# Kernel optimization log

Measured on AMD Instinct MI355X. Metric: run time of the kernel, lower is better.

The kernel has to match this reference:

```python
import jax, jax.numpy as jnp
import numpy as np

D_MODEL = 512
NUM_HEADS = 8
DEPTH = D_MODEL // NUM_HEADS
BATCH = 16
SEQ = 1024


def setup_inputs() -> dict:
    key = jax.random.key(0)
    kq, kk, kv, k1, k2, k3, k4 = jax.random.split(key, 7)
    scale = 1.0 / np.sqrt(D_MODEL)
    return {
        "v": jax.random.normal(kv, (BATCH, SEQ, D_MODEL), jnp.float32),
        "k": jax.random.normal(kk, (BATCH, SEQ, D_MODEL), jnp.float32),
        "q": jax.random.normal(kq, (BATCH, SEQ, D_MODEL), jnp.float32),
        "mask": jnp.ones((BATCH, SEQ), jnp.float32),
        # Conv1D(kernel_size=1, use_bias=False) == per-token Linear: x @ W, W [d_in, d_out]
        "Wq": jax.random.normal(k1, (D_MODEL, D_MODEL), jnp.float32) * scale,
        "Wk": jax.random.normal(k2, (D_MODEL, D_MODEL), jnp.float32) * scale,
        "Wv": jax.random.normal(k3, (D_MODEL, D_MODEL), jnp.float32) * scale,
        "Wo": jax.random.normal(k4, (D_MODEL, D_MODEL), jnp.float32) * scale,
    }


def _split_heads(x, batch):
    # [b, s, d_model] -> [b, h, s, depth]
    return x.reshape(batch, -1, NUM_HEADS, DEPTH).transpose(0, 2, 1, 3)


def reference(v, k, q, mask, Wq, Wk, Wv, Wo):
    batch = q.shape[0]
    qh = _split_heads(q @ Wq, batch)  # [b,h,sq,dh]
    kh = _split_heads(k @ Wk, batch)  # [b,h,sk,dh]
    vh = _split_heads(v @ Wv, batch)  # [b,h,sk,dh]

    dk = jnp.asarray(DEPTH, qh.dtype)
    logits = jnp.einsum("bhqd,bhkd->bhqk", qh, kh) / jnp.sqrt(dk)
    # additive padding mask, broadcast [b,1,1,sk]
    logits = logits + (1.0 - mask[:, None, None, :]) * (-1e9)
    attention_weights = jax.nn.softmax(logits, axis=-1)  # [b,h,sq,sk]

    ctx = jnp.einsum("bhqk,bhkd->bhqd", attention_weights, vh)
    ctx = ctx.transpose(0, 2, 1, 3).reshape(batch, -1, D_MODEL)
    output = ctx @ Wo
    return output, attention_weights
```

## Files before the change

### kernel.cpp

```cpp
#include <hip/hip_runtime.h>


typedef _Float16 f16;
typedef _Float16 f16x8 __attribute__((ext_vector_type(8)));
typedef float f32x4 __attribute__((ext_vector_type(4)));

#define DEVINL __device__ __forceinline__

static constexpr int BATCH = 16, SEQ = 1024, DM = 512, NH = 8, DH = 64;

DEVINL void async16(void* lds, const void* g) {
  __builtin_amdgcn_global_load_lds(
      (const __attribute__((address_space(1))) unsigned int*)g,
      (__attribute__((address_space(3))) unsigned int*)lds, 16, 0, 0);
}

__global__ __launch_bounds__(256) void prep_wt_k(
    const float* __restrict__ Wq, const float* __restrict__ Wk,
    const float* __restrict__ Wv, const float* __restrict__ Wo,
    f16* __restrict__ WT) {
  __shared__ float t[32][33];
  const int w = blockIdx.z;
  const float* src = (w == 0) ? Wq : (w == 1) ? Wk : (w == 2) ? Wv : Wo;
  const int k0 = blockIdx.y * 32, n0 = blockIdx.x * 32;
  const int r0 = threadIdx.x >> 5, c = threadIdx.x & 31;
#pragma unroll
  for (int i = 0; i < 4; ++i)
    t[i * 8 + r0][c] = src[(size_t)(k0 + i * 8 + r0) * DM + n0 + c];
  __syncthreads();
  f16* dst = WT + (size_t)w * DM * DM;
#pragma unroll
  for (int i = 0; i < 4; ++i)
    dst[(size_t)(n0 + i * 8 + r0) * DM + k0 + c] = (f16)t[c][i * 8 + r0];
}

template <int MODE>
DEVINL void gemm_body(const float* __restrict__ A32, const f16* __restrict__ A16,
                      const f16* __restrict__ WTn, f16* __restrict__ O16,
                      float* __restrict__ O32) {
  __shared__ __align__(16) f16 As[128 * 32];
  __shared__ __align__(16) f16 Bs[128 * 32];
  const int tid = threadIdx.x;
  const int lane = tid & 63, wave = tid >> 6;
  const int wr = wave >> 1, wc = wave & 1;
  const int m0 = blockIdx.x * 128, n0 = blockIdx.y * 128;
  const int lrow = lane & 15, lkg = lane >> 4;
  f32x4 acc[4][4] = {};

  for (int kt = 0; kt < DM / 32; ++kt) {
    const int k0 = kt * 32;
#pragma unroll
    for (int it = 0; it < 2; ++it) {
      const int o = (it * 256 + tid) * 16;
      const int n = o >> 6, kb = o & 63;
      async16((char*)Bs + (it * 256 + wave * 64) * 16,
              (const char*)WTn + ((size_t)(n0 + n) * DM + k0) * 2 + kb);
    }
    if (MODE == 0) {
      const int row = tid >> 1, kh = (tid & 1) * 16;
      const float* s = A32 + (size_t)(m0 + row) * DM + k0 + kh;
#pragma unroll
      for (int half = 0; half < 2; ++half) {
        f32x4 v0 = *(const f32x4*)(s + half * 8);
        f32x4 v1 = *(const f32x4*)(s + half * 8 + 4);
        f16x8 t;
        t[0] = (f16)v0[0]; t[1] = (f16)v0[1]; t[2] = (f16)v0[2]; t[3] = (f16)v0[3];
        t[4] = (f16)v1[0]; t[5] = (f16)v1[1]; t[6] = (f16)v1[2]; t[7] = (f16)v1[3];
        *(f16x8*)&As[row * 32 + kh + half * 8] = t;
      }
    } else {
#pragma unroll
      for (int it = 0; it < 2; ++it) {
        const int o = (it * 256 + tid) * 16;
        const int row = o >> 6, kb = o & 63;
        async16((char*)As + (it * 256 + wave * 64) * 16,
                (const char*)A16 + ((size_t)(m0 + row) * DM + k0) * 2 + kb);
      }
    }
    __syncthreads();
    f16x8 af[4], bf[4];
#pragma unroll
    for (int i = 0; i < 4; ++i)
      af[i] = *(const f16x8*)&As[(wr * 64 + i * 16 + lrow) * 32 + lkg * 8];
#pragma unroll
    for (int j = 0; j < 4; ++j)
      bf[j] = *(const f16x8*)&Bs[(wc * 64 + j * 16 + lrow) * 32 + lkg * 8];
#pragma unroll
    for (int i = 0; i < 4; ++i)
#pragma unroll
      for (int j = 0; j < 4; ++j)
        acc[i][j] = __builtin_amdgcn_mfma_f32_16x16x32_f16(af[i], bf[j], acc[i][j], 0, 0, 0);
    __syncthreads();
  }

#pragma unroll
  for (int i = 0; i < 4; ++i) {
#pragma unroll
    for (int j = 0; j < 4; ++j) {
#pragma unroll
      for (int r = 0; r < 4; ++r) {
        const int m = m0 + wr * 64 + i * 16 + lkg * 4 + r;
        const int g = n0 + wc * 64 + j * 16 + lrow;
        if (MODE == 0) {
          const int b = m >> 10, s = m & 1023, hh = g >> 6, d = g & 63;
          O16[(((size_t)b * NH + hh) * SEQ + s) * DH + d] = (f16)acc[i][j][r];
        } else {
          O32[(size_t)m * DM + g] = acc[i][j][r];
        }
      }
    }
  }
}

__global__ __launch_bounds__(256, 2) void proj_k(
    const float* __restrict__ q, const float* __restrict__ k, const float* __restrict__ v,
    const f16* __restrict__ WT, f16* __restrict__ Qh, f16* __restrict__ Kh,
    f16* __restrict__ Vh) {
  const int z = blockIdx.z;
  const float* A = (z == 0) ? q : (z == 1) ? k : v;
  const f16* W = WT + (size_t)z * DM * DM;
  f16* O = (z == 0) ? Qh : (z == 1) ? Kh : Vh;
  gemm_body<0>(A, nullptr, W, O, nullptr);
}

__global__ __launch_bounds__(256, 2) void outp_k(const f16* __restrict__ ctx,
                                                 const f16* __restrict__ WoT,
                                                 float* __restrict__ out0) {
  gemm_body<1>(nullptr, ctx, WoT, nullptr, out0);
}

__global__ __launch_bounds__(256, 2) void attn_k(
    const f16* __restrict__ Qh, const f16* __restrict__ Kh, const f16* __restrict__ Vh,
    const float* __restrict__ mask, float* __restrict__ attnW, f16* __restrict__ ctx) {
  __shared__ __align__(16) f16 Ks[64 * 64];
  __shared__ __align__(16) f16 Vt[64 * 64];
  __shared__ __align__(16) f16 Ps[4][16 * 64];
  const int tid = threadIdx.x;
  const int lane = tid & 63, wave = tid >> 6;
  const int lrow = lane & 15, lkg = lane >> 4;
  const int qt = blockIdx.x, h = blockIdx.y, b = blockIdx.z;
  const size_t bh = (size_t)b * NH + h;
  const f16* Kbase = Kh + bh * SEQ * DH;
  const f16* Vbase = Vh + bh * SEQ * DH;
  const int q0 = qt * 64 + wave * 16;

  f16x8 aQ0, aQ1;
  {
    const f16* qp = Qh + (bh * SEQ + q0 + lrow) * DH + lkg * 8;
    aQ0 = *(const f16x8*)qp;
    aQ1 = *(const f16x8*)(qp + 32);
  }

  float sums[4] = {0.f, 0.f, 0.f, 0.f};

  for (int kt = 0; kt < 16; ++kt) {
    const char* KtileB = (const char*)(Kbase + (size_t)kt * 64 * DH);
#pragma unroll
    for (int it = 0; it < 2; ++it) {
      const int o = (it * 256 + tid) * 16;
      const int key = o >> 7, slot = (o >> 4) & 7;
      async16((char*)Ks + (it * 256 + wave * 64) * 16,
              KtileB + key * 128 + ((slot ^ (key & 7)) << 4));
    }
    __syncthreads();
    f32x4 lg[4] = {};
#pragma unroll
    for (int j = 0; j < 4; ++j) {
      const int key = j * 16 + lrow;
      f16x8 b0 = *(const f16x8*)((const char*)Ks + key * 128 + ((lkg ^ (key & 7)) << 4));
      f16x8 b1 = *(const f16x8*)((const char*)Ks + key * 128 + (((4 + lkg) ^ (key & 7)) << 4));
      lg[j] = __builtin_amdgcn_mfma_f32_16x16x32_f16(aQ0, b0, lg[j], 0, 0, 0);
      lg[j] = __builtin_amdgcn_mfma_f32_16x16x32_f16(aQ1, b1, lg[j], 0, 0, 0);
    }
#pragma unroll
    for (int j = 0; j < 4; ++j) {
      const int key = kt * 64 + j * 16 + lrow;
      const float bias = (1.0f - mask[b * SEQ + key]) * (-1e9f);
#pragma unroll
      for (int r = 0; r < 4; ++r) sums[r] += __expf(lg[j][r] * 0.125f + bias);
    }
    __syncthreads();
  }

#pragma unroll
  for (int r = 0; r < 4; ++r) {
    float s = sums[r];
    s += __shfl_xor(s, 1);
    s += __shfl_xor(s, 2);
    s += __shfl_xor(s, 4);
    s += __shfl_xor(s, 8);
    sums[r] = 1.0f / s;
  }

  f32x4 ctxacc[4] = {};
  float* awBase = attnW + (bh * SEQ + q0) * SEQ;

  for (int kt = 0; kt < 16; ++kt) {
    const char* KtileB = (const char*)(Kbase + (size_t)kt * 64 * DH);
#pragma unroll
    for (int it = 0; it < 2; ++it) {
      const int o = (it * 256 + tid) * 16;
      const int key = o >> 7, slot = (o >> 4) & 7;
      async16((char*)Ks + (it * 256 + wave * 64) * 16,
              KtileB + key * 128 + ((slot ^ (key & 7)) << 4));
    }
    {
      const int key = tid >> 2, d0 = (tid & 3) * 16;
      const f16* vp = Vbase + ((size_t)kt * 64 + key) * DH + d0;
      f16x8 v0 = *(const f16x8*)vp;
      f16x8 v1 = *(const f16x8*)(vp + 8);
#pragma unroll
      for (int jj = 0; jj < 8; ++jj) {
        const int d = d0 + jj;
        *(f16*)((char*)Vt + d * 128 + (((key >> 3) ^ (d & 7)) << 4) + (key & 7) * 2) = v0[jj];
      }
#pragma unroll
      for (int jj = 0; jj < 8; ++jj) {
        const int d = d0 + 8 + jj;
        *(f16*)((char*)Vt + d * 128 + (((key >> 3) ^ (d & 7)) << 4) + (key & 7) * 2) = v1[jj];
      }
    }
    __syncthreads();
    f32x4 lg[4] = {};
#pragma unroll
    for (int j = 0; j < 4; ++j) {
      const int key = j * 16 + lrow;
      f16x8 b0 = *(const f16x8*)((const char*)Ks + key * 128 + ((lkg ^ (key & 7)) << 4));
      f16x8 b1 = *(const f16x8*)((const char*)Ks + key * 128 + (((4 + lkg) ^ (key & 7)) << 4));
      lg[j] = __builtin_amdgcn_mfma_f32_16x16x32_f16(aQ0, b0, lg[j], 0, 0, 0);
      lg[j] = __builtin_amdgcn_mfma_f32_16x16x32_f16(aQ1, b1, lg[j], 0, 0, 0);
    }
    float* aw = awBase + kt * 64;
#pragma unroll
    for (int j = 0; j < 4; ++j) {
      const int keyc = j * 16 + lrow;
      const float bias = (1.0f - mask[b * SEQ + kt * 64 + keyc]) * (-1e9f);
#pragma unroll
      for (int r = 0; r < 4; ++r) {
        const int row = lkg * 4 + r;
        const float w = __expf(lg[j][r] * 0.125f + bias) * sums[r];
        aw[(size_t)row * SEQ + keyc] = w;
        *(f16*)((char*)&Ps[wave][0] + row * 128 + (((keyc >> 3) ^ (row & 7)) << 4) +
                (keyc & 7) * 2) = (f16)w;
      }
    }
#pragma unroll
    for (int kk = 0; kk < 2; ++kk) {
      const int kidx = kk * 32 + lkg * 8;
      f16x8 aP = *(const f16x8*)((const char*)&Ps[wave][0] + lrow * 128 +
                                 (((kidx >> 3) ^ (lrow & 7)) << 4));
#pragma unroll
      for (int j2 = 0; j2 < 4; ++j2) {
        const int d = j2 * 16 + lrow;
        f16x8 bV = *(const f16x8*)((const char*)Vt + d * 128 + (((kidx >> 3) ^ (d & 7)) << 4));
        ctxacc[j2] = __builtin_amdgcn_mfma_f32_16x16x32_f16(aP, bV, ctxacc[j2], 0, 0, 0);
      }
    }
    __syncthreads();
  }

#pragma unroll
  for (int j2 = 0; j2 < 4; ++j2)
#pragma unroll
    for (int r = 0; r < 4; ++r) {
      const int s = q0 + lkg * 4 + r;
      const int d = j2 * 16 + lrow;
      ctx[(((size_t)b * SEQ + s) * NH + h) * DH + d] = (f16)ctxacc[j2][r];
    }
}

extern "C" void kernel_launch(void* const* d_in, const int* in_sizes, int n_in,
                              void* d_out, int out_size, void* d_ws, size_t ws_size,
                              hipStream_t stream) {
  const float* v = (const float*)d_in[0];
  const float* k = (const float*)d_in[1];
  const float* q = (const float*)d_in[2];
  const float* mask = (const float*)d_in[3];
  const float* Wq = (const float*)d_in[4];
  const float* Wk = (const float*)d_in[5];
  const float* Wv = (const float*)d_in[6];
  const float* Wo = (const float*)d_in[7];

  float* out0 = (float*)d_out;
  float* attnW = out0 + (size_t)BATCH * SEQ * DM;

  char* ws = (char*)d_ws;
  f16* WT = (f16*)ws;
  f16* Qh = (f16*)(ws + (size_t)4 * DM * DM * 2);
  f16* Kh = Qh + (size_t)BATCH * NH * SEQ * DH;
  f16* Vh = Kh + (size_t)BATCH * NH * SEQ * DH;
  f16* ctx = Vh + (size_t)BATCH * NH * SEQ * DH;

  prep_wt_k<<<dim3(16, 16, 4), 256, 0, stream>>>(Wq, Wk, Wv, Wo, WT);
  proj_k<<<dim3(128, 4, 3), 256, 0, stream>>>(q, k, v, WT, Qh, Kh, Vh);
  attn_k<<<dim3(16, NH, BATCH), 256, 0, stream>>>(Qh, Kh, Vh, mask, attnW, ctx);
  outp_k<<<dim3(128, 4), 256, 0, stream>>>(ctx, WT + (size_t)3 * DM * DM, out0);
}
```

Before: 313.2 us.

## Double-buffer LDS tiles in GEMMs and attention, remap blocks for XCD locality

Adds double-buffered LDS staging to the projection GEMMs and to both attention passes. The next K/V or A/B tile is prefetched, asynchronously or into registers, while MFMAs run on the current one, which also drops one barrier per iteration. Launches become 1D grids whose block ids are remapped so consecutive work lands on the same XCD (bid&7 striding), aiming for better L2 reuse of K/V and weights. LDS use doubles, which could reduce occupancy. The attention kernel is likely dominated by the 64MB attention-weight writes, which limits what overlap can gain.

```diff
diff --git a/kernel.cpp b/kernel.cpp
--- a/kernel.cpp
+++ b/kernel.cpp
@@ -37,59 +37,85 @@
 template <int MODE>
 DEVINL void gemm_body(const float* __restrict__ A32, const f16* __restrict__ A16,
                       const f16* __restrict__ WTn, f16* __restrict__ O16,
-                      float* __restrict__ O32) {
-  __shared__ __align__(16) f16 As[128 * 32];
-  __shared__ __align__(16) f16 Bs[128 * 32];
+                      float* __restrict__ O32, int m0, int n0) {
+  __shared__ __align__(16) f16 As[2][128 * 32];
+  __shared__ __align__(16) f16 Bs[2][128 * 32];
   const int tid = threadIdx.x;
   const int lane = tid & 63, wave = tid >> 6;
   const int wr = wave >> 1, wc = wave & 1;
-  const int m0 = blockIdx.x * 128, n0 = blockIdx.y * 128;
   const int lrow = lane & 15, lkg = lane >> 4;
   f32x4 acc[4][4] = {};
 
-  for (int kt = 0; kt < DM / 32; ++kt) {
-    const int k0 = kt * 32;
+  f32x4 ar[4];
+
+  auto stageB = [&](int kt, int buf) {
 #pragma unroll
     for (int it = 0; it < 2; ++it) {
       const int o = (it * 256 + tid) * 16;
       const int n = o >> 6, kb = o & 63;
-      async16((char*)Bs + (it * 256 + wave * 64) * 16,
-              (const char*)WTn + ((size_t)(n0 + n) * DM + k0) * 2 + kb);
-    }
-    if (MODE == 0) {
-      const int row = tid >> 1, kh = (tid & 1) * 16;
-      const float* s = A32 + (size_t)(m0 + row) * DM + k0 + kh;
-#pragma unroll
-      for (int half = 0; half < 2; ++half) {
-        f32x4 v0 = *(const f32x4*)(s + half * 8);
-        f32x4 v1 = *(const f32x4*)(s + half * 8 + 4);
-        f16x8 t;
-        t[0] = (f16)v0[0]; t[1] = (f16)v0[1]; t[2] = (f16)v0[2]; t[3] = (f16)v0[3];
-        t[4] = (f16)v1[0]; t[5] = (f16)v1[1]; t[6] = (f16)v1[2]; t[7] = (f16)v1[3];
-        *(f16x8*)&As[row * 32 + kh + half * 8] = t;
-      }
-    } else {
-#pragma unroll
-      for (int it = 0; it < 2; ++it) {
-        const int o = (it * 256 + tid) * 16;
-        const int row = o >> 6, kb = o & 63;
-        async16((char*)As + (it * 256 + wave * 64) * 16,
-                (const char*)A16 + ((size_t)(m0 + row) * DM + k0) * 2 + kb);
-      }
-    }
-    __syncthreads();
+      async16((char*)&Bs[buf][0] + (it * 256 + wave * 64) * 16,
+              (const char*)WTn + ((size_t)(n0 + n) * DM + kt * 32) * 2 + kb);
+    }
+  };
+  auto stageA_async = [&](int kt, int buf) {
+#pragma unroll
+    for (int it = 0; it < 2; ++it) {
+      const int o = (it * 256 + tid) * 16;
+      const int row = o >> 6, kb = o & 63;
+      async16((char*)&As[buf][0] + (it * 256 + wave * 64) * 16,
+              (const char*)A16 + ((size_t)(m0 + row) * DM + kt * 32) * 2 + kb);
+    }
+  };
+  auto loadA = [&](int kt) {
+    const int row = tid >> 1, kh = (tid & 1) * 16;
+    const float* s = A32 + (size_t)(m0 + row) * DM + kt * 32 + kh;
+    ar[0] = *(const f32x4*)(s);
+    ar[1] = *(const f32x4*)(s + 4);
+    ar[2] = *(const f32x4*)(s + 8);
+    ar[3] = *(const f32x4*)(s + 12);
+  };
+  auto writeA = [&](int buf) {
+    const int row = tid >> 1, kh = (tid & 1) * 16;
+#pragma unroll
+    for (int half = 0; half < 2; ++half) {
+      f16x8 t;
+      t[0] = (f16)ar[half * 2][0]; t[1] = (f16)ar[half * 2][1];
+      t[2] = (f16)ar[half * 2][2]; t[3] = (f16)ar[half * 2][3];
+      t[4] = (f16)ar[half * 2 + 1][0]; t[5] = (f16)ar[half * 2 + 1][1];
+      t[6] = (f16)ar[half * 2 + 1][2]; t[7] = (f16)ar[half * 2 + 1][3];
+      *(f16x8*)&As[buf][row * 32 + kh + half * 8] = t;
+    }
+  };
+
+  stageB(0, 0);
+  if (MODE == 0) {
+    loadA(0);
+    writeA(0);
+  } else {
+    stageA_async(0, 0);
+  }
+  __syncthreads();
+
+  for (int kt = 0; kt < DM / 32; ++kt) {
+    const int cur = kt & 1;
+    if (kt < DM / 32 - 1) {
+      stageB(kt + 1, cur ^ 1);
+      if (MODE == 0) loadA(kt + 1);
+      else stageA_async(kt + 1, cur ^ 1);
+    }
     f16x8 af[4], bf[4];
 #pragma unroll
     for (int i = 0; i < 4; ++i)
-      af[i] = *(const f16x8*)&As[(wr * 64 + i * 16 + lrow) * 32 + lkg * 8];
+      af[i] = *(const f16x8*)&As[cur][(wr * 64 + i * 16 + lrow) * 32 + lkg * 8];
 #pragma unroll
     for (int j = 0; j < 4; ++j)
-      bf[j] = *(const f16x8*)&Bs[(wc * 64 + j * 16 + lrow) * 32 + lkg * 8];
+      bf[j] = *(const f16x8*)&Bs[cur][(wc * 64 + j * 16 + lrow) * 32 + lkg * 8];
 #pragma unroll
     for (int i = 0; i < 4; ++i)
 #pragma unroll
       for (int j = 0; j < 4; ++j)
         acc[i][j] = __builtin_amdgcn_mfma_f32_16x16x32_f16(af[i], bf[j], acc[i][j], 0, 0, 0);
+    if (MODE == 0 && kt < DM / 32 - 1) writeA(cur ^ 1);
     __syncthreads();
   }
 
@@ -116,33 +142,51 @@
     const float* __restrict__ q, const float* __restrict__ k, const float* __restrict__ v,
     const f16* __restrict__ WT, f16* __restrict__ Qh, f16* __restrict__ Kh,
     f16* __restrict__ Vh) {
-  const int z = blockIdx.z;
+  const int bid = blockIdx.x;
+  const int wid = (bid & 7) * 192 + (bid >> 3);
+  const int n_blk = wid & 3, m_blk = (wid >> 2) & 127, z = wid >> 9;
   const float* A = (z == 0) ? q : (z == 1) ? k : v;
   const f16* W = WT + (size_t)z * DM * DM;
   f16* O = (z == 0) ? Qh : (z == 1) ? Kh : Vh;
-  gemm_body<0>(A, nullptr, W, O, nullptr);
+  gemm_body<0>(A, nullptr, W, O, nullptr, m_blk * 128, n_blk * 128);
 }
 
 __global__ __launch_bounds__(256, 2) void outp_k(const f16* __restrict__ ctx,
                                                  const f16* __restrict__ WoT,
                                                  float* __restrict__ out0) {
-  gemm_body<1>(nullptr, ctx, WoT, nullptr, out0);
+  const int bid = blockIdx.x;
+  const int wid = (bid & 7) * 64 + (bid >> 3);
+  const int n_blk = wid & 3, m_blk = wid >> 2;
+  gemm_body<1>(nullptr, ctx, WoT, nullptr, out0, m_blk * 128, n_blk * 128);
 }
 
 __global__ __launch_bounds__(256, 2) void attn_k(
     const f16* __restrict__ Qh, const f16* __restrict__ Kh, const f16* __restrict__ Vh,
     const float* __restrict__ mask, float* __restrict__ attnW, f16* __restrict__ ctx) {
-  __shared__ __align__(16) f16 Ks[64 * 64];
-  __shared__ __align__(16) f16 Vt[64 * 64];
+  __shared__ __align__(16) f16 Ks[2][64 * 64];
+  __shared__ __align__(16) f16 Vt[2][64 * 64];
   __shared__ __align__(16) f16 Ps[4][16 * 64];
   const int tid = threadIdx.x;
   const int lane = tid & 63, wave = tid >> 6;
   const int lrow = lane & 15, lkg = lane >> 4;
-  const int qt = blockIdx.x, h = blockIdx.y, b = blockIdx.z;
+  const int bid = blockIdx.x;
+  const int wid = (bid & 7) * 256 + (bid >> 3);
+  const int qt = wid & 15, h = (wid >> 4) & 7, b = wid >> 7;
   const size_t bh = (size_t)b * NH + h;
   const f16* Kbase = Kh + bh * SEQ * DH;
   const f16* Vbase = Vh + bh * SEQ * DH;
   const int q0 = qt * 64 + wave * 16;
+
+  auto stageK = [&](int kt, int buf) {
+    const char* KtileB = (const char*)(Kbase + (size_t)kt * 64 * DH);
+#pragma unroll
+    for (int it = 0; it < 2; ++it) {
+      const int o = (it * 256 + tid) * 16;
+      const int key = o >> 7, slot = (o >> 4) & 7;
+      async16((char*)&Ks[buf][0] + (it * 256 + wave * 64) * 16,
+              KtileB + key * 128 + ((slot ^ (key & 7)) << 4));
+    }
+  };
 
   f16x8 aQ0, aQ1;
   {
@@ -153,22 +197,17 @@
 
   float sums[4] = {0.f, 0.f, 0.f, 0.f};
 
+  stageK(0, 0);
+  __syncthreads();
   for (int kt = 0; kt < 16; ++kt) {
-    const char* KtileB = (const char*)(Kbase + (size_t)kt * 64 * DH);
-#pragma unroll
-    for (int it = 0; it < 2; ++it) {
-      const int o = (it * 256 + tid) * 16;
-      const int key = o >> 7, slot = (o >> 4) & 7;
-      async16((char*)Ks + (it * 256 + wave * 64) * 16,
-              KtileB + key * 128 + ((slot ^ (key & 7)) << 4));
-    }
-    __syncthreads();
+    const int cur = kt & 1;
+    if (kt < 15) stageK(kt + 1, cur ^ 1);
     f32x4 lg[4] = {};
 #pragma unroll
     for (int j = 0; j < 4; ++j) {
       const int key = j * 16 + lrow;
-      f16x8 b0 = *(const f16x8*)((const char*)Ks + key * 128 + ((lkg ^ (key & 7)) << 4));
-      f16x8 b1 = *(const f16x8*)((const char*)Ks + key * 128 + (((4 + lkg) ^ (key & 7)) << 4));
+      f16x8 b0 = *(const f16x8*)((const char*)&Ks[cur][0] + key * 128 + ((lkg ^ (key & 7)) << 4));
+      f16x8 b1 = *(const f16x8*)((const char*)&Ks[cur][0] + key * 128 + (((4 + lkg) ^ (key & 7)) << 4));
       lg[j] = __builtin_amdgcn_mfma_f32_16x16x32_f16(aQ0, b0, lg[j], 0, 0, 0);
       lg[j] = __builtin_amdgcn_mfma_f32_16x16x32_f16(aQ1, b1, lg[j], 0, 0, 0);
     }
@@ -195,38 +234,42 @@
   f32x4 ctxacc[4] = {};
   float* awBase = attnW + (bh * SEQ + q0) * SEQ;
 
+  const int vkey = tid >> 2, vd0 = (tid & 3) * 16;
+  f16x8 vr0, vr1;
+  auto loadV = [&](int kt) {
+    const f16* vp = Vbase + ((size_t)kt * 64 + vkey) * DH + vd0;
+    vr0 = *(const f16x8*)vp;
+    vr1 = *(const f16x8*)(vp + 8);
+  };
+  auto writeVt = [&](int buf) {
+#pragma unroll
+    for (int jj = 0; jj < 8; ++jj) {
+      const int d = vd0 + jj;
+      *(f16*)((char*)&Vt[buf][0] + d * 128 + (((vkey >> 3) ^ (d & 7)) << 4) + (vkey & 7) * 2) = vr0[jj];
+    }
+#pragma unroll
+    for (int jj = 0; jj < 8; ++jj) {
+      const int d = vd0 + 8 + jj;
+      *(f16*)((char*)&Vt[buf][0] + d * 128 + (((vkey >> 3) ^ (d & 7)) << 4) + (vkey & 7) * 2) = vr1[jj];
+    }
+  };
+
+  stageK(0, 0);
+  loadV(0);
+  writeVt(0);
+  __syncthreads();
   for (int kt = 0; kt < 16; ++kt) {
-    const char* KtileB = (const char*)(Kbase + (size_t)kt * 64 * DH);
-#pragma unroll
-    for (int it = 0; it < 2; ++it) {
-      const int o = (it * 256 + tid) * 16;
-      const int key = o >> 7, slot = (o >> 4) & 7;
-      async16((char*)Ks + (it * 256 + wave * 64) * 16,
-              KtileB + key * 128 + ((slot ^ (key & 7)) << 4));
-    }
-    {
-      const int key = tid >> 2, d0 = (tid & 3) * 16;
-      const f16* vp = Vbase + ((size_t)kt * 64 + key) * DH + d0;
-      f16x8 v0 = *(const f16x8*)vp;
-      f16x8 v1 = *(const f16x8*)(vp + 8);
-#pragma unroll
-      for (int jj = 0; jj < 8; ++jj) {
-        const int d = d0 + jj;
-        *(f16*)((char*)Vt + d * 128 + (((key >> 3) ^ (d & 7)) << 4) + (key & 7) * 2) = v0[jj];
-      }
-#pragma unroll
-      for (int jj = 0; jj < 8; ++jj) {
-        const int d = d0 + 8 + jj;
-        *(f16*)((char*)Vt + d * 128 + (((key >> 3) ^ (d & 7)) << 4) + (key & 7) * 2) = v1[jj];
-      }
-    }
-    __syncthreads();
+    const int cur = kt & 1;
+    if (kt < 15) {
+      stageK(kt + 1, cur ^ 1);
+      loadV(kt + 1);
+    }
     f32x4 lg[4] = {};
 #pragma unroll
     for (int j = 0; j < 4; ++j) {
       const int key = j * 16 + lrow;
-      f16x8 b0 = *(const f16x8*)((const char*)Ks + key * 128 + ((lkg ^ (key & 7)) << 4));
-      f16x8 b1 = *(const f16x8*)((const char*)Ks + key * 128 + (((4 + lkg) ^ (key & 7)) << 4));
+      f16x8 b0 = *(const f16x8*)((const char*)&Ks[cur][0] + key * 128 + ((lkg ^ (key & 7)) << 4));
+      f16x8 b1 = *(const f16x8*)((const char*)&Ks[cur][0] + key * 128 + (((4 + lkg) ^ (key & 7)) << 4));
       lg[j] = __builtin_amdgcn_mfma_f32_16x16x32_f16(aQ0, b0, lg[j], 0, 0, 0);
       lg[j] = __builtin_amdgcn_mfma_f32_16x16x32_f16(aQ1, b1, lg[j], 0, 0, 0);
     }
@@ -252,10 +295,11 @@
 #pragma unroll
       for (int j2 = 0; j2 < 4; ++j2) {
         const int d = j2 * 16 + lrow;
-        f16x8 bV = *(const f16x8*)((const char*)Vt + d * 128 + (((kidx >> 3) ^ (d & 7)) << 4));
+        f16x8 bV = *(const f16x8*)((const char*)&Vt[cur][0] + d * 128 + (((kidx >> 3) ^ (d & 7)) << 4));
         ctxacc[j2] = __builtin_amdgcn_mfma_f32_16x16x32_f16(aP, bV, ctxacc[j2], 0, 0, 0);
       }
     }
+    if (kt < 15) writeVt(cur ^ 1);
     __syncthreads();
   }
 
@@ -292,7 +336,7 @@
   f16* ctx = Vh + (size_t)BATCH * NH * SEQ * DH;
 
   prep_wt_k<<<dim3(16, 16, 4), 256, 0, stream>>>(Wq, Wk, Wv, Wo, WT);
-  proj_k<<<dim3(128, 4, 3), 256, 0, stream>>>(q, k, v, WT, Qh, Kh, Vh);
-  attn_k<<<dim3(16, NH, BATCH), 256, 0, stream>>>(Qh, Kh, Vh, mask, attnW, ctx);
-  outp_k<<<dim3(128, 4), 256, 0, stream>>>(ctx, WT + (size_t)3 * DM * DM, out0);
-}
+  proj_k<<<dim3(1536), 256, 0, stream>>>(q, k, v, WT, Qh, Kh, Vh);
+  attn_k<<<dim3(2048), 256, 0, stream>>>(Qh, Kh, Vh, mask, attnW, ctx);
+  outp_k<<<dim3(512), 256, 0, stream>>>(ctx, WT + (size_t)3 * DM * DM, out0);
+}
```

After: 319.7 us. 1.02x slower.
